# Kernel tuning notes

Measured on AMD Instinct MI355X. Metric: run time of the kernel, lower is better.

The kernel has to match this reference:

```python
import jax, jax.numpy as jnp
import numpy as np

INPUT_DIM = 50
OUTPUT_DIM = 50


def setup_inputs() -> dict:
    key = jax.random.key(0)
    k1, k2, k3, k4 = jax.random.split(key, 4)
    B, N = 512, 256
    nfm = jax.random.normal(k1, (B, N, INPUT_DIM), dtype=jnp.float32)
    efm = jax.random.uniform(k2, (B, N, N), dtype=jnp.float32)
    # Linear params (torch nn.Linear default init: U(-1/sqrt(fan_in), 1/sqrt(fan_in)))
    bound = 1.0 / np.sqrt(INPUT_DIM)
    W = jax.random.uniform(k3, (OUTPUT_DIM, INPUT_DIM), dtype=jnp.float32, minval=-bound, maxval=bound)
    b = jax.random.uniform(k4, (OUTPUT_DIM,), dtype=jnp.float32, minval=-bound, maxval=bound)
    return {"nfm": nfm, "efm": efm, "W": W, "b": b}


def reference(nfm, efm, W, b):
    # x = bmm(efm, nfm): [B, N, N] @ [B, N, D] -> [B, N, D]
    x = jnp.einsum("bnm,bmd->bnd", efm, nfm)
    # Linear + ReLU (epilogue)
    return jax.nn.relu(jnp.einsum("bnd,od->bno", x, W) + b)
```

## Files before the change

kernel.cpp:

```cpp
#include <hip/hip_runtime.h>
#include <hip/hip_bf16.h>


typedef float f32x4 __attribute__((ext_vector_type(4)));
typedef short s16x8 __attribute__((ext_vector_type(8)));

#define TPB 512

__device__ __forceinline__ unsigned short f2bf(float f) {
    union { float f; unsigned u; } a; a.f = f;
    unsigned u = a.u;
    unsigned rounded = u + 0x7fffu + ((u >> 16) & 1u);
    return (unsigned short)(rounded >> 16);
}

__global__ __launch_bounds__(TPB, 4)
void gconv_fused(const float* __restrict__ nfm,
                 const float* __restrict__ efm,
                 const float* __restrict__ W,
                 const float* __restrict__ bias,
                 float* __restrict__ out)
{
    __shared__ unsigned short nfm_s[256 * 72];
    __shared__ unsigned short w_s[64 * 72];
    __shared__ unsigned short z_s[64 * 264];

    const int tid   = threadIdx.x;
    const int lane  = tid & 63;
    const int wv    = tid >> 6;
    const int col16 = lane & 15;
    const int kg    = lane >> 4;
    const int kg8   = kg * 8;
    const int b     = blockIdx.x;

    const float* nfm_b = nfm + (size_t)b * (256 * 50);
    const float* efm_b = efm + (size_t)b * (256 * 256);
    float*       out_b = out + (size_t)b * (256 * 50);

    {
        unsigned* p = (unsigned*)nfm_s;
        for (int i = tid; i < 256 * 72 / 2; i += TPB) p[i] = 0u;
        unsigned* q = (unsigned*)w_s;
        for (int i = tid; i < 64 * 72 / 2; i += TPB) q[i] = 0u;
    }
    __syncthreads();

    for (int i = tid; i < 3200; i += TPB) {
        f32x4 v = *(const f32x4*)(nfm_b + i * 4);
        int e = i * 4;
        #pragma unroll
        for (int j = 0; j < 4; ++j) {
            int r = (e + j) / 50, k = (e + j) % 50;
            nfm_s[r * 72 + k] = f2bf(v[j]);
        }
    }
    for (int i = tid; i < 625; i += TPB) {
        f32x4 v = *(const f32x4*)(W + i * 4);
        int e = i * 4;
        #pragma unroll
        for (int j = 0; j < 4; ++j) {
            int o = (e + j) / 50, k = (e + j) % 50;
            w_s[o * 72 + k] = f2bf(v[j]);
        }
    }

    float bia[4];
    #pragma unroll
    for (int ot = 0; ot < 4; ++ot) {
        int c = ot * 16 + col16;
        bia[ot] = (c < 50) ? bias[c] : 0.f;
    }
    __syncthreads();

    {
        s16x8 wf[2][4];
        #pragma unroll
        for (int kk = 0; kk < 2; ++kk)
            #pragma unroll
            for (int ot = 0; ot < 4; ++ot)
                wf[kk][ot] = *(const s16x8*)&w_s[(ot * 16 + col16) * 72 + kk * 32 + kg8];

        #pragma unroll
        for (int mt = 0; mt < 2; ++mt) {
            int row = wv * 32 + mt * 16 + col16;
            s16x8 a0 = *(const s16x8*)&nfm_s[row * 72 + kg8];
            s16x8 a1 = *(const s16x8*)&nfm_s[row * 72 + 32 + kg8];
            #pragma unroll
            for (int ot = 0; ot < 4; ++ot) {
                f32x4 acc = {0.f, 0.f, 0.f, 0.f};
                acc = __builtin_amdgcn_mfma_f32_16x16x32_bf16(a0, wf[0][ot], acc, 0, 0, 0);
                acc = __builtin_amdgcn_mfma_f32_16x16x32_bf16(a1, wf[1][ot], acc, 0, 0, 0);
                #pragma unroll
                for (int r = 0; r < 4; ++r) {
                    int m = wv * 32 + mt * 16 + kg * 4 + r;
                    int o = ot * 16 + col16;
                    z_s[o * 264 + m] = f2bf(acc[r]);
                }
            }
        }
    }
    __syncthreads();

    f32x4 acc[2][4];
    #pragma unroll
    for (int mt = 0; mt < 2; ++mt)
        #pragma unroll
        for (int ot = 0; ot < 4; ++ot)
            acc[mt][ot] = (f32x4){0.f, 0.f, 0.f, 0.f};

    const int wrow = wv * 32;
    #pragma unroll
    for (int ks = 0; ks < 8; ++ks) {
        s16x8 bf[4];
        #pragma unroll
        for (int ot = 0; ot < 4; ++ot)
            bf[ot] = *(const s16x8*)&z_s[(ot * 16 + col16) * 264 + ks * 32 + kg8];
        #pragma unroll
        for (int mt = 0; mt < 2; ++mt) {
            const float* ap = efm_b + (wrow + mt * 16 + col16) * 256 + ks * 32 + kg8;
            f32x4 lo = *(const f32x4*)ap;
            f32x4 hi = *(const f32x4*)(ap + 4);
            s16x8 af;
            #pragma unroll
            for (int j = 0; j < 4; ++j) {
                af[j]     = (short)f2bf(lo[j]);
                af[4 + j] = (short)f2bf(hi[j]);
            }
            #pragma unroll
            for (int ot = 0; ot < 4; ++ot)
                acc[mt][ot] = __builtin_amdgcn_mfma_f32_16x16x32_bf16(af, bf[ot], acc[mt][ot], 0, 0, 0);
        }
    }

    #pragma unroll
    for (int mt = 0; mt < 2; ++mt)
        #pragma unroll
        for (int ot = 0; ot < 4; ++ot) {
            int o = ot * 16 + col16;
            if (o < 50) {
                #pragma unroll
                for (int r = 0; r < 4; ++r) {
                    int n = wrow + mt * 16 + kg * 4 + r;
                    out_b[n * 50 + o] = fmaxf(acc[mt][ot][r] + bia[ot], 0.f);
                }
            }
        }
}

extern "C" void kernel_launch(void* const* d_in, const int* in_sizes, int n_in,
                              void* d_out, int out_size, void* d_ws, size_t ws_size,
                              hipStream_t stream) {
    const float* nfm  = (const float*)d_in[0];
    const float* efm  = (const float*)d_in[1];
    const float* W    = (const float*)d_in[2];
    const float* bias = (const float*)d_in[3];
    float* out = (float*)d_out;

    gconv_fused<<<dim3(512), dim3(TPB), 0, stream>>>(nfm, efm, W, bias, out);
}
```

Baseline: 225.6 us.

## Split fused kernel into Z precompute and row-tiled efm GEMM with prefetch

Splits the fused kernel into two launches when workspace is large enough. The first computes Z = nfm·Wᵀ per batch in bf16 and writes it to workspace. The second runs 1024 blocks of 256 threads, each covering half the rows of one batch. It stages Z into LDS with global_load_lds, software-prefetches efm tiles one k-step ahead, and uses the builtin bf16 conversion. This aims to raise the number of blocks in flight and hide efm load latency, at the cost of an extra launch and a Z round-trip through global memory.

```diff
diff --git a/kernel.cpp b/kernel.cpp
--- a/kernel.cpp
+++ b/kernel.cpp
@@ -5,7 +5,12 @@
 typedef float f32x4 __attribute__((ext_vector_type(4)));
 typedef short s16x8 __attribute__((ext_vector_type(8)));
 
-#define TPB 512
+#define AS1C(p) ((const __attribute__((address_space(1))) unsigned int*)(p))
+#define AS3(p)  ((__attribute__((address_space(3))) unsigned int*)(p))
+
+#define Z_STRIDE 264
+#define Z_ELEMS  (64 * Z_STRIDE)
+#define Z_CHUNKS (Z_ELEMS * 2 / 16)
 
 __device__ __forceinline__ unsigned short f2bf(float f) {
     union { float f; unsigned u; } a; a.f = f;
@@ -14,16 +19,25 @@
     return (unsigned short)(rounded >> 16);
 }
 
-__global__ __launch_bounds__(TPB, 4)
-void gconv_fused(const float* __restrict__ nfm,
-                 const float* __restrict__ efm,
-                 const float* __restrict__ W,
-                 const float* __restrict__ bias,
-                 float* __restrict__ out)
+__device__ __forceinline__ s16x8 cvt8(f32x4 lo, f32x4 hi) {
+    s16x8 r;
+    #pragma unroll
+    for (int j = 0; j < 4; ++j) {
+        __hip_bfloat16 x = __float2bfloat16(lo[j]);
+        __hip_bfloat16 y = __float2bfloat16(hi[j]);
+        r[j]     = __builtin_bit_cast(short, x);
+        r[4 + j] = __builtin_bit_cast(short, y);
+    }
+    return r;
+}
+
+__global__ __launch_bounds__(256, 4)
+void compute_z(const float* __restrict__ nfm, const float* __restrict__ W,
+               unsigned short* __restrict__ zws)
 {
     __shared__ unsigned short nfm_s[256 * 72];
     __shared__ unsigned short w_s[64 * 72];
-    __shared__ unsigned short z_s[64 * 264];
+    __shared__ unsigned short z_s[Z_ELEMS];
 
     const int tid   = threadIdx.x;
     const int lane  = tid & 63;
@@ -32,20 +46,185 @@
     const int kg    = lane >> 4;
     const int kg8   = kg * 8;
     const int b     = blockIdx.x;
-
+    const float* nfm_b = nfm + (size_t)b * (256 * 50);
+
+    {
+        unsigned* p = (unsigned*)nfm_s;
+        for (int i = tid; i < 256 * 72 / 2; i += 256) p[i] = 0u;
+        unsigned* q = (unsigned*)w_s;
+        for (int i = tid; i < 64 * 72 / 2; i += 256) q[i] = 0u;
+    }
+    __syncthreads();
+
+    for (int i = tid; i < 3200; i += 256) {
+        f32x4 v = *(const f32x4*)(nfm_b + i * 4);
+        int e = i * 4;
+        #pragma unroll
+        for (int j = 0; j < 4; ++j) {
+            int r = (e + j) / 50, k = (e + j) % 50;
+            nfm_s[r * 72 + k] = f2bf(v[j]);
+        }
+    }
+    for (int i = tid; i < 625; i += 256) {
+        f32x4 v = *(const f32x4*)(W + i * 4);
+        int e = i * 4;
+        #pragma unroll
+        for (int j = 0; j < 4; ++j) {
+            int o = (e + j) / 50, k = (e + j) % 50;
+            w_s[o * 72 + k] = f2bf(v[j]);
+        }
+    }
+    __syncthreads();
+
+    s16x8 wf[2][4];
+    #pragma unroll
+    for (int kk = 0; kk < 2; ++kk)
+        #pragma unroll
+        for (int ot = 0; ot < 4; ++ot)
+            wf[kk][ot] = *(const s16x8*)&w_s[(ot * 16 + col16) * 72 + kk * 32 + kg8];
+
+    #pragma unroll
+    for (int mt = 0; mt < 4; ++mt) {
+        int row = wv * 64 + mt * 16 + col16;
+        s16x8 a0 = *(const s16x8*)&nfm_s[row * 72 + kg8];
+        s16x8 a1 = *(const s16x8*)&nfm_s[row * 72 + 32 + kg8];
+        #pragma unroll
+        for (int ot = 0; ot < 4; ++ot) {
+            f32x4 acc = {0.f, 0.f, 0.f, 0.f};
+            acc = __builtin_amdgcn_mfma_f32_16x16x32_bf16(a0, wf[0][ot], acc, 0, 0, 0);
+            acc = __builtin_amdgcn_mfma_f32_16x16x32_bf16(a1, wf[1][ot], acc, 0, 0, 0);
+            #pragma unroll
+            for (int r = 0; r < 4; ++r) {
+                int m = wv * 64 + mt * 16 + kg * 4 + r;
+                int o = ot * 16 + col16;
+                z_s[o * Z_STRIDE + m] = f2bf(acc[r]);
+            }
+        }
+    }
+    __syncthreads();
+
+    uint4* dst = (uint4*)(zws + (size_t)b * Z_ELEMS);
+    const uint4* src = (const uint4*)z_s;
+    for (int i = tid; i < Z_CHUNKS; i += 256) dst[i] = src[i];
+}
+
+__global__ __launch_bounds__(256, 4)
+void gemm_out(const float* __restrict__ efm,
+              const unsigned short* __restrict__ zws,
+              const float* __restrict__ bias,
+              float* __restrict__ out)
+{
+    __shared__ unsigned short z_s[Z_ELEMS];
+
+    const int tid   = threadIdx.x;
+    const int lane  = tid & 63;
+    const int wv    = tid >> 6;
+    const int col16 = lane & 15;
+    const int kg    = lane >> 4;
+    const int kg8   = kg * 8;
+    const int bid   = blockIdx.x;
+    const int b     = bid >> 1;
+    const int rt    = bid & 1;
+
+    const unsigned short* zb = zws + (size_t)b * Z_ELEMS;
+    #pragma unroll
+    for (int i = 0; i < 9; ++i) {
+        int idx = i * 256 + tid;
+        if (idx < Z_CHUNKS) {
+            __builtin_amdgcn_global_load_lds(
+                AS1C((const char*)zb + (size_t)idx * 16),
+                AS3((char*)z_s + (i * 256 + wv * 64) * 16), 16, 0, 0);
+        }
+    }
+
+    float bia[4];
+    #pragma unroll
+    for (int ot = 0; ot < 4; ++ot) {
+        int c = ot * 16 + col16;
+        bia[ot] = (c < 50) ? bias[c] : 0.f;
+    }
+    __syncthreads();
+
+    const float* efm_b = efm + (size_t)b * (256 * 256);
+    float*       out_b = out + (size_t)b * (256 * 50);
+    const int r0 = rt * 128 + wv * 32;
+
+    f32x4 acc[2][4];
+    #pragma unroll
+    for (int mt = 0; mt < 2; ++mt)
+        #pragma unroll
+        for (int ot = 0; ot < 4; ++ot)
+            acc[mt][ot] = (f32x4){0.f, 0.f, 0.f, 0.f};
+
+    const float* ap0 = efm_b + (r0 + col16) * 256 + kg8;
+    const float* ap1 = efm_b + (r0 + 16 + col16) * 256 + kg8;
+
+    f32x4 lo0 = *(const f32x4*)ap0, hi0 = *(const f32x4*)(ap0 + 4);
+    f32x4 lo1 = *(const f32x4*)ap1, hi1 = *(const f32x4*)(ap1 + 4);
+
+    #pragma unroll
+    for (int ks = 0; ks < 8; ++ks) {
+        f32x4 nlo0, nhi0, nlo1, nhi1;
+        if (ks < 7) {
+            const float* p0 = ap0 + (ks + 1) * 32;
+            const float* p1 = ap1 + (ks + 1) * 32;
+            nlo0 = *(const f32x4*)p0; nhi0 = *(const f32x4*)(p0 + 4);
+            nlo1 = *(const f32x4*)p1; nhi1 = *(const f32x4*)(p1 + 4);
+        }
+        s16x8 bf[4];
+        #pragma unroll
+        for (int ot = 0; ot < 4; ++ot)
+            bf[ot] = *(const s16x8*)&z_s[(ot * 16 + col16) * Z_STRIDE + ks * 32 + kg8];
+
+        s16x8 a0 = cvt8(lo0, hi0);
+        s16x8 a1 = cvt8(lo1, hi1);
+        #pragma unroll
+        for (int ot = 0; ot < 4; ++ot) {
+            acc[0][ot] = __builtin_amdgcn_mfma_f32_16x16x32_bf16(a0, bf[ot], acc[0][ot], 0, 0, 0);
+            acc[1][ot] = __builtin_amdgcn_mfma_f32_16x16x32_bf16(a1, bf[ot], acc[1][ot], 0, 0, 0);
+        }
+        lo0 = nlo0; hi0 = nhi0; lo1 = nlo1; hi1 = nhi1;
+    }
+
+    #pragma unroll
+    for (int mt = 0; mt < 2; ++mt)
+        #pragma unroll
+        for (int ot = 0; ot < 4; ++ot) {
+            int o = ot * 16 + col16;
+            if (o < 50) {
+                #pragma unroll
+                for (int r = 0; r < 4; ++r) {
+                    int n = r0 + mt * 16 + kg * 4 + r;
+                    out_b[n * 50 + o] = fmaxf(acc[mt][ot][r] + bia[ot], 0.f);
+                }
+            }
+        }
+}
+
+__global__ __launch_bounds__(512, 4)
+void gconv_fused(const float* __restrict__ nfm, const float* __restrict__ efm,
+                 const float* __restrict__ W, const float* __restrict__ bias,
+                 float* __restrict__ out)
+{
+    __shared__ unsigned short nfm_s[256 * 72];
+    __shared__ unsigned short w_s[64 * 72];
+    __shared__ unsigned short z_s[64 * 264];
+
+    const int tid = threadIdx.x, lane = tid & 63, wv = tid >> 6;
+    const int col16 = lane & 15, kg = lane >> 4, kg8 = kg * 8;
+    const int b = blockIdx.x;
     const float* nfm_b = nfm + (size_t)b * (256 * 50);
     const float* efm_b = efm + (size_t)b * (256 * 256);
     float*       out_b = out + (size_t)b * (256 * 50);
 
     {
         unsigned* p = (unsigned*)nfm_s;
-        for (int i = tid; i < 256 * 72 / 2; i += TPB) p[i] = 0u;
+        for (int i = tid; i < 256 * 72 / 2; i += 512) p[i] = 0u;
         unsigned* q = (unsigned*)w_s;
-        for (int i = tid; i < 64 * 72 / 2; i += TPB) q[i] = 0u;
-    }
-    __syncthreads();
-
-    for (int i = tid; i < 3200; i += TPB) {
+        for (int i = tid; i < 64 * 72 / 2; i += 512) q[i] = 0u;
+    }
+    __syncthreads();
+    for (int i = tid; i < 3200; i += 512) {
         f32x4 v = *(const f32x4*)(nfm_b + i * 4);
         int e = i * 4;
         #pragma unroll
@@ -54,7 +233,7 @@
             nfm_s[r * 72 + k] = f2bf(v[j]);
         }
     }
-    for (int i = tid; i < 625; i += TPB) {
+    for (int i = tid; i < 625; i += 512) {
         f32x4 v = *(const f32x4*)(W + i * 4);
         int e = i * 4;
         #pragma unroll
@@ -63,7 +242,6 @@
             w_s[o * 72 + k] = f2bf(v[j]);
         }
     }
-
     float bia[4];
     #pragma unroll
     for (int ot = 0; ot < 4; ++ot) {
@@ -71,7 +249,6 @@
         bia[ot] = (c < 50) ? bias[c] : 0.f;
     }
     __syncthreads();
-
     {
         s16x8 wf[2][4];
         #pragma unroll
@@ -79,7 +256,6 @@
             #pragma unroll
             for (int ot = 0; ot < 4; ++ot)
                 wf[kk][ot] = *(const s16x8*)&w_s[(ot * 16 + col16) * 72 + kk * 32 + kg8];
-
         #pragma unroll
         for (int mt = 0; mt < 2; ++mt) {
             int row = wv * 32 + mt * 16 + col16;
@@ -91,23 +267,18 @@
                 acc = __builtin_amdgcn_mfma_f32_16x16x32_bf16(a0, wf[0][ot], acc, 0, 0, 0);
                 acc = __builtin_amdgcn_mfma_f32_16x16x32_bf16(a1, wf[1][ot], acc, 0, 0, 0);
                 #pragma unroll
-                for (int r = 0; r < 4; ++r) {
-                    int m = wv * 32 + mt * 16 + kg * 4 + r;
-                    int o = ot * 16 + col16;
-                    z_s[o * 264 + m] = f2bf(acc[r]);
-                }
+                for (int r = 0; r < 4; ++r)
+                    z_s[(ot * 16 + col16) * 264 + wv * 32 + mt * 16 + kg * 4 + r] = f2bf(acc[r]);
             }
         }
     }
     __syncthreads();
-
     f32x4 acc[2][4];
     #pragma unroll
     for (int mt = 0; mt < 2; ++mt)
         #pragma unroll
         for (int ot = 0; ot < 4; ++ot)
             acc[mt][ot] = (f32x4){0.f, 0.f, 0.f, 0.f};
-
     const int wrow = wv * 32;
     #pragma unroll
     for (int ks = 0; ks < 8; ++ks) {
@@ -120,18 +291,12 @@
             const float* ap = efm_b + (wrow + mt * 16 + col16) * 256 + ks * 32 + kg8;
             f32x4 lo = *(const f32x4*)ap;
             f32x4 hi = *(const f32x4*)(ap + 4);
-            s16x8 af;
-            #pragma unroll
-            for (int j = 0; j < 4; ++j) {
-                af[j]     = (short)f2bf(lo[j]);
-                af[4 + j] = (short)f2bf(hi[j]);
-            }
+            s16x8 af = cvt8(lo, hi);
             #pragma unroll
             for (int ot = 0; ot < 4; ++ot)
                 acc[mt][ot] = __builtin_amdgcn_mfma_f32_16x16x32_bf16(af, bf[ot], acc[mt][ot], 0, 0, 0);
         }
     }
-
     #pragma unroll
     for (int mt = 0; mt < 2; ++mt)
         #pragma unroll
@@ -156,5 +321,12 @@
     const float* bias = (const float*)d_in[3];
     float* out = (float*)d_out;
 
-    gconv_fused<<<dim3(512), dim3(TPB), 0, stream>>>(nfm, efm, W, bias, out);
-}
+    const size_t need = (size_t)512 * Z_ELEMS * sizeof(unsigned short);
+    if (ws_size >= need) {
+        unsigned short* zws = (unsigned short*)d_ws;
+        compute_z<<<dim3(512), dim3(256), 0, stream>>>(nfm, W, zws);
+        gemm_out<<<dim3(1024), dim3(256), 0, stream>>>(efm, zws, bias, out);
+    } else {
+        gconv_fused<<<dim3(512), dim3(512), 0, stream>>>(nfm, efm, W, bias, out);
+    }
+}
```

After: 239.0 us. 1.06x slower.

## Prefetch efm tiles, swizzle LDS layout, and pack bf16 stores

Applied to the files above, without the earlier changes.

Loads the first efm tile before the shared-memory setup, then double-buffers the efm register loads one k-step ahead inside the main MFMA loop. This hides global-memory latency behind compute. It also replaces the padded 72-stride LDS layout for nfm and W with an XOR-swizzled 64-stride layout to avoid bank conflicts, packs pairs of bf16 values into 32-bit stores when writing z_s, and switches to the library bf16 conversion. The cost is higher register pressure from the prefetch buffers, which may hurt occupancy under the 4-block launch bound.

```diff
diff --git a/kernel.cpp b/kernel.cpp
--- a/kernel.cpp
+++ b/kernel.cpp
@@ -8,21 +8,37 @@
 #define TPB 512
 
 __device__ __forceinline__ unsigned short f2bf(float f) {
-    union { float f; unsigned u; } a; a.f = f;
-    unsigned u = a.u;
-    unsigned rounded = u + 0x7fffu + ((u >> 16) & 1u);
-    return (unsigned short)(rounded >> 16);
+    __hip_bfloat16 h = __float2bfloat16(f);
+    return __builtin_bit_cast(unsigned short, h);
+}
+
+__device__ __forceinline__ unsigned bfpair(float a, float b) {
+    return (unsigned)f2bf(a) | ((unsigned)f2bf(b) << 16);
+}
+
+__device__ __forceinline__ s16x8 cvt8(f32x4 lo, f32x4 hi) {
+    s16x8 r;
+    #pragma unroll
+    for (int j = 0; j < 4; ++j) {
+        r[j]     = (short)f2bf(lo[j]);
+        r[4 + j] = (short)f2bf(hi[j]);
+    }
+    return r;
+}
+
+__device__ __forceinline__ int swz(int row, int k) {
+    return row * 64 + ((((k >> 3) ^ (row & 7)) << 3) | (k & 7));
 }
 
 __global__ __launch_bounds__(TPB, 4)
-void gconv_fused(const float* __restrict__ nfm,
-                 const float* __restrict__ efm,
-                 const float* __restrict__ W,
-                 const float* __restrict__ bias,
-                 float* __restrict__ out)
+void gconv_v3(const float* __restrict__ nfm,
+              const float* __restrict__ efm,
+              const float* __restrict__ W,
+              const float* __restrict__ bias,
+              float* __restrict__ out)
 {
-    __shared__ unsigned short nfm_s[256 * 72];
-    __shared__ unsigned short w_s[64 * 72];
+    __shared__ unsigned short nfm_p[256 * 64];
+    __shared__ unsigned short w_s[64 * 64];
     __shared__ unsigned short z_s[64 * 264];
 
     const int tid   = threadIdx.x;
@@ -37,11 +53,19 @@
     const float* efm_b = efm + (size_t)b * (256 * 256);
     float*       out_b = out + (size_t)b * (256 * 50);
 
+    const int r0 = wv * 32;
+    const float* ap0 = efm_b + (r0 + col16) * 256 + kg8;
+    const float* ap1 = efm_b + (r0 + 16 + col16) * 256 + kg8;
+    f32x4 lo0 = *(const f32x4*)ap0, hi0 = *(const f32x4*)(ap0 + 4);
+    f32x4 lo1 = *(const f32x4*)ap1, hi1 = *(const f32x4*)(ap1 + 4);
+
     {
-        unsigned* p = (unsigned*)nfm_s;
-        for (int i = tid; i < 256 * 72 / 2; i += TPB) p[i] = 0u;
+        unsigned* p = (unsigned*)nfm_p;
+        #pragma unroll
+        for (int i = 0; i < 16; ++i) p[i * TPB + tid] = 0u;
         unsigned* q = (unsigned*)w_s;
-        for (int i = tid; i < 64 * 72 / 2; i += TPB) q[i] = 0u;
+        #pragma unroll
+        for (int i = 0; i < 4; ++i) q[i * TPB + tid] = 0u;
     }
     __syncthreads();
 
@@ -51,7 +75,7 @@
         #pragma unroll
         for (int j = 0; j < 4; ++j) {
             int r = (e + j) / 50, k = (e + j) % 50;
-            nfm_s[r * 72 + k] = f2bf(v[j]);
+            nfm_p[swz(r, k)] = f2bf(v[j]);
         }
     }
     for (int i = tid; i < 625; i += TPB) {
@@ -60,7 +84,7 @@
         #pragma unroll
         for (int j = 0; j < 4; ++j) {
             int o = (e + j) / 50, k = (e + j) % 50;
-            w_s[o * 72 + k] = f2bf(v[j]);
+            w_s[swz(o, k)] = f2bf(v[j]);
         }
     }
 
@@ -77,25 +101,25 @@
         #pragma unroll
         for (int kk = 0; kk < 2; ++kk)
             #pragma unroll
-            for (int ot = 0; ot < 4; ++ot)
-                wf[kk][ot] = *(const s16x8*)&w_s[(ot * 16 + col16) * 72 + kk * 32 + kg8];
-
+            for (int ot = 0; ot < 4; ++ot) {
+                int o = ot * 16 + col16;
+                wf[kk][ot] = *(const s16x8*)&w_s[o * 64 + ((((kk << 2) | kg) ^ (o & 7)) << 3)];
+            }
         #pragma unroll
         for (int mt = 0; mt < 2; ++mt) {
             int row = wv * 32 + mt * 16 + col16;
-            s16x8 a0 = *(const s16x8*)&nfm_s[row * 72 + kg8];
-            s16x8 a1 = *(const s16x8*)&nfm_s[row * 72 + 32 + kg8];
+            int r7  = row & 7;
+            s16x8 a0 = *(const s16x8*)&nfm_p[row * 64 + ((kg ^ r7) << 3)];
+            s16x8 a1 = *(const s16x8*)&nfm_p[row * 64 + (((4 | kg) ^ r7) << 3)];
             #pragma unroll
             for (int ot = 0; ot < 4; ++ot) {
                 f32x4 acc = {0.f, 0.f, 0.f, 0.f};
                 acc = __builtin_amdgcn_mfma_f32_16x16x32_bf16(a0, wf[0][ot], acc, 0, 0, 0);
                 acc = __builtin_amdgcn_mfma_f32_16x16x32_bf16(a1, wf[1][ot], acc, 0, 0, 0);
-                #pragma unroll
-                for (int r = 0; r < 4; ++r) {
-                    int m = wv * 32 + mt * 16 + kg * 4 + r;
-                    int o = ot * 16 + col16;
-                    z_s[o * 264 + m] = f2bf(acc[r]);
-                }
+                int m = wv * 32 + mt * 16 + kg * 4;
+                int o = ot * 16 + col16;
+                *(unsigned*)&z_s[o * 264 + m]     = bfpair(acc[0], acc[1]);
+                *(unsigned*)&z_s[o * 264 + m + 2] = bfpair(acc[2], acc[3]);
             }
         }
     }
@@ -108,28 +132,28 @@
         for (int ot = 0; ot < 4; ++ot)
             acc[mt][ot] = (f32x4){0.f, 0.f, 0.f, 0.f};
 
-    const int wrow = wv * 32;
     #pragma unroll
     for (int ks = 0; ks < 8; ++ks) {
+        f32x4 nlo0, nhi0, nlo1, nhi1;
+        if (ks < 7) {
+            const float* p0 = ap0 + (ks + 1) * 32;
+            const float* p1 = ap1 + (ks + 1) * 32;
+            nlo0 = *(const f32x4*)p0; nhi0 = *(const f32x4*)(p0 + 4);
+            nlo1 = *(const f32x4*)p1; nhi1 = *(const f32x4*)(p1 + 4);
+        }
         s16x8 bf[4];
         #pragma unroll
         for (int ot = 0; ot < 4; ++ot)
             bf[ot] = *(const s16x8*)&z_s[(ot * 16 + col16) * 264 + ks * 32 + kg8];
+
+        s16x8 a0 = cvt8(lo0, hi0);
+        s16x8 a1 = cvt8(lo1, hi1);
         #pragma unroll
-        for (int mt = 0; mt < 2; ++mt) {
-            const float* ap = efm_b + (wrow + mt * 16 + col16) * 256 + ks * 32 + kg8;
-            f32x4 lo = *(const f32x4*)ap;
-            f32x4 hi = *(const f32x4*)(ap + 4);
-            s16x8 af;
-            #pragma unroll
-            for (int j = 0; j < 4; ++j) {
-                af[j]     = (short)f2bf(lo[j]);
-                af[4 + j] = (short)f2bf(hi[j]);
-            }
-            #pragma unroll
-            for (int ot = 0; ot < 4; ++ot)
-                acc[mt][ot] = __builtin_amdgcn_mfma_f32_16x16x32_bf16(af, bf[ot], acc[mt][ot], 0, 0, 0);
+        for (int ot = 0; ot < 4; ++ot) {
+            acc[0][ot] = __builtin_amdgcn_mfma_f32_16x16x32_bf16(a0, bf[ot], acc[0][ot], 0, 0, 0);
+            acc[1][ot] = __builtin_amdgcn_mfma_f32_16x16x32_bf16(a1, bf[ot], acc[1][ot], 0, 0, 0);
         }
+        lo0 = nlo0; hi0 = nhi0; lo1 = nlo1; hi1 = nhi1;
     }
 
     #pragma unroll
@@ -140,7 +164,7 @@
             if (o < 50) {
                 #pragma unroll
                 for (int r = 0; r < 4; ++r) {
-                    int n = wrow + mt * 16 + kg * 4 + r;
+                    int n = r0 + mt * 16 + kg * 4 + r;
                     out_b[n * 50 + o] = fmaxf(acc[mt][ot][r] + bia[ot], 0.f);
                 }
             }
@@ -156,5 +180,5 @@
     const float* bias = (const float*)d_in[3];
     float* out = (float*)d_out;
 
-    gconv_fused<<<dim3(512), dim3(TPB), 0, stream>>>(nfm, efm, W, bias, out);
+    gconv_v3<<<dim3(512), dim3(TPB), 0, stream>>>(nfm, efm, W, bias, out);
 }
```

After: 227.6 us. About the same (+0.9%).
